# Kernel optimization log

Measured on AMD Instinct MI355X. Metric: run time of the kernel, lower is better.

Reference implementation:

```python
import jax, jax.numpy as jnp
import numpy as np

VOCAB = 1000
HID = 512      # hidden_size == context_size (hidden is initialized to context)
EMB = 512


def setup_inputs() -> dict:
    key = jax.random.key(0)
    ks = jax.random.split(key, 8)
    B = 128
    scale_ih = 1.0 / np.sqrt(HID)
    inp = {
        "context": jax.random.normal(ks[0], (B, HID), dtype=jnp.float32),
        "embed_table": jax.random.normal(ks[1], (VOCAB, EMB), dtype=jnp.float32) * 0.02,
        "W_ih": jax.random.uniform(ks[2], (4 * HID, HID + EMB), minval=-scale_ih, maxval=scale_ih, dtype=jnp.float32),
        "b_ih": jax.random.uniform(ks[3], (4 * HID,), minval=-scale_ih, maxval=scale_ih, dtype=jnp.float32),
        "W_hh": jax.random.uniform(ks[4], (4 * HID, HID), minval=-scale_ih, maxval=scale_ih, dtype=jnp.float32),
        "b_hh": jax.random.uniform(ks[5], (4 * HID,), minval=-scale_ih, maxval=scale_ih, dtype=jnp.float32),
        "W_out": jax.random.uniform(ks[6], (VOCAB, HID), minval=-scale_ih, maxval=scale_ih, dtype=jnp.float32),
        "b_out": jax.random.uniform(ks[7], (VOCAB,), minval=-scale_ih, maxval=scale_ih, dtype=jnp.float32),
        "start_id": 1,
        "max_seq_len": 256,
    }
    return inp


def reference(context, embed_table, W_ih, b_ih, W_hh, b_hh, W_out, b_out, start_id, max_seq_len):
    B = context.shape[0]
    hidden0 = context                                   # torch: hidden = context
    cell0 = jnp.zeros((B, HID), dtype=context.dtype)
    init_emb = jnp.broadcast_to(embed_table[start_id], (B, EMB))

    def step(carry, _):
        h, c, emb = carry
        x = jnp.concatenate([context, emb], axis=1)     # [B, C+E]
        gates = x @ W_ih.T + b_ih + h @ W_hh.T + b_hh   # [B, 4H]
        i_g, f_g, g_g, o_g = jnp.split(gates, 4, axis=1)  # torch LSTMCell gate order
        i_g = jax.nn.sigmoid(i_g)
        f_g = jax.nn.sigmoid(f_g)
        g_g = jnp.tanh(g_g)
        o_g = jax.nn.sigmoid(o_g)
        c_new = f_g * c + i_g * g_g
        h_new = o_g * jnp.tanh(c_new)
        out = h_new @ W_out.T + b_out                   # [B, V]
        next_emb = embed_table[jnp.argmax(out, axis=1)]  # greedy-decode feedback
        return (h_new, c_new, next_emb), out

    (h_f, c_f, _), outs = jax.lax.scan(step, (hidden0, cell0, init_emb), None, length=max_seq_len)
    output_tensor = jnp.transpose(outs, (1, 0, 2))      # [B, T, V]
    return output_tensor, h_f, c_f
```

## Files before the change

### kernel.cpp

```cpp
#include <hip/hip_runtime.h>
#include <float.h>
#include <math.h>

#define B_    128
#define H_    512
#define V_    1000
#define T_    256
#define G4_   2048
#define NBLK  256
#define SPIN_MAX (1 << 17)

#define AT_LOAD(p)    __hip_atomic_load((p), __ATOMIC_RELAXED, __HIP_MEMORY_SCOPE_AGENT)
#define AT_STORE(p,v) __hip_atomic_store((p), (v), __ATOMIC_RELAXED, __HIP_MEMORY_SCOPE_AGENT)

typedef float f2 __attribute__((ext_vector_type(2)));

#define PINF2(v_) asm volatile("" : "+v"(v_))

__device__ __forceinline__ float red4(float x) {
  x += __int_as_float(__builtin_amdgcn_mov_dpp(__float_as_int(x), 0xB1, 0xF, 0xF, true));
  x += __int_as_float(__builtin_amdgcn_mov_dpp(__float_as_int(x), 0x4E, 0xF, 0xF, true));
  return x;
}

__device__ __forceinline__ float fsigmoid(float x) {
  return 1.f / (1.f + __expf(-x));
}
__device__ __forceinline__ float ftanh(float x) {
  const float e = __expf(2.f * fabsf(x));
  return copysignf(1.f - 2.f / (e + 1.f), x);
}

__global__ __launch_bounds__(256) void gemm_nt_k512(
    const float* __restrict__ A, int M,
    const float* __restrict__ Bm, int ldb, int koff,
    const float* __restrict__ bias1, const float* __restrict__ bias2,
    float* __restrict__ C, int ldc, int ileave)
{
  __shared__ float As[16][68];
  __shared__ float Bs[16][68];
  const int tid = threadIdx.x;
  const int m0 = blockIdx.y * 64, n0 = blockIdx.x * 64;
  const int tm = tid & 15, tn = tid >> 4;
  const int lm = tid & 63, kq = tid >> 6;
  float acc[4][4] = {};
  for (int k0 = 0; k0 < 512; k0 += 16) {
    float4 av = make_float4(0.f, 0.f, 0.f, 0.f);
    if (m0 + lm < M) av = *(const float4*)(A + (size_t)(m0 + lm) * 512 + k0 + kq * 4);
    float4 bv = *(const float4*)(Bm + (size_t)(n0 + lm) * ldb + koff + k0 + kq * 4);
    __syncthreads();
    As[kq*4+0][lm] = av.x; As[kq*4+1][lm] = av.y; As[kq*4+2][lm] = av.z; As[kq*4+3][lm] = av.w;
    Bs[kq*4+0][lm] = bv.x; Bs[kq*4+1][lm] = bv.y; Bs[kq*4+2][lm] = bv.z; Bs[kq*4+3][lm] = bv.w;
    __syncthreads();
#pragma unroll
    for (int kk = 0; kk < 16; ++kk) {
      const float4 a = *(const float4*)&As[kk][tm * 4];
      const float4 b = *(const float4*)&Bs[kk][tn * 4];
      const float aa[4] = {a.x, a.y, a.z, a.w};
      const float bb[4] = {b.x, b.y, b.z, b.w};
#pragma unroll
      for (int i = 0; i < 4; ++i)
#pragma unroll
        for (int j = 0; j < 4; ++j)
          acc[i][j] = fmaf(aa[i], bb[j], acc[i][j]);
    }
  }
#pragma unroll
  for (int i = 0; i < 4; ++i) {
    const int m = m0 + tm * 4 + i;
    if (m < M) {
#pragma unroll
      for (int j = 0; j < 4; ++j) {
        const int n = n0 + tn * 4 + j;
        float v = acc[i][j];
        if (bias1) v += bias1[n];
        if (bias2) v += bias2[n];
        const size_t idx = ileave ? ((size_t)m * ldc + (size_t)(n & 511) * 4 + (n >> 9))
                                  : ((size_t)m * ldc + n);
        C[idx] = v;
      }
    }
  }
}

__global__ __launch_bounds__(256) void init_kernel(
    const float* __restrict__ ctx, float* __restrict__ hbuf,
    unsigned long long* __restrict__ amax,
    int* __restrict__ hdone, const int* __restrict__ start_id)
{
  const int i = blockIdx.x * blockDim.x + threadIdx.x;
  ((float4*)(hbuf + B_ * H_))[i] = ((const float4*)ctx)[i];
  if (i < B_ * 32) {
    const int m = i & 31;
    const unsigned long long w = (m == 0)
        ? ((((unsigned long long)__float_as_uint(FLT_MAX)) << 32) |
           (1u << 16) | (unsigned)(*start_id))
        : ((((unsigned long long)__float_as_uint(-FLT_MAX)) << 32) | (1u << 16));
    amax[(size_t)B_ * 32 + i] = w;
  }
  if (i < 2 * 8 * 32) hdone[i * 16] = 0;
}

__global__ __launch_bounds__(512, 2) void decoder_main(
    const float* __restrict__ Whh,
    const float* __restrict__ Wout,
    const float* __restrict__ bout,
    const float* __restrict__ proj,
    const float* __restrict__ basep,
    float* __restrict__ hbuf,
    unsigned long long* __restrict__ amax,
    int* __restrict__ hdone,
    float* __restrict__ out)
{
  __shared__ struct alignas(16) SM {
    float hs[16][640];
    float gbase[16][68];
    float gq[2][16][324];
    float lq[2][16][132];
    float sbout[32];
    int   tok[16];
  } sm;

  const int tid  = threadIdx.x;
  const int bid  = blockIdx.x;
  const int gid  = bid >> 5;
  const int mem  = bid & 31;
  const int lane = tid & 63;
  const int w    = tid >> 6;
  const int row_base = gid * 16;
  const int vb   = mem * 32;

  const int q1  = lane >> 4;
  const int kc  = lane & 15;
  const int i3  = kc & 3;
  const int quad = kc >> 2;
  const int blk = w & 3;
  const int par = w >> 2;
  const int hoff  = par * 256 + kc * 16;
  const int hcol  = (par * 16 + kc) * 20;

  const int goff = (q1 * 4 + i3) * 20 + blk * 4 + quad;
  const int loff = (blk * 8 + q1 * 2 + i3) * 4 + quad;

  f2 w1p[4][8];
#pragma unroll
  for (int i = 0; i < 4; ++i) {
    const f2* p = (const f2*)(Whh + (size_t)(blk * 512 + mem * 16 + q1 * 4 + i) * H_ + hoff);
#pragma unroll
    for (int j = 0; j < 8; ++j) w1p[i][j] = p[j];
  }
  const int v0 = vb + blk * 8 + q1 * 2;
  f2 w2p[2][8];
#pragma unroll
  for (int jj = 0; jj < 2; ++jj) {
    const int vv = (v0 + jj < V_) ? (v0 + jj) : (V_ - 1);
    const f2* p = (const f2*)(Wout + (size_t)vv * H_ + hoff);
#pragma unroll
    for (int j = 0; j < 8; ++j) w2p[jj][j] = p[j];
  }
#pragma unroll
  for (int i = 0; i < 4; ++i)
#pragma unroll
    for (int j = 0; j < 8; ++j) PINF2(w1p[i][j]);
#pragma unroll
  for (int jj = 0; jj < 2; ++jj)
#pragma unroll
    for (int j = 0; j < 8; ++j) PINF2(w2p[jj][j]);

#pragma unroll
  for (int kx = 0; kx < 2; ++kx) {
    const int e = tid + kx * 512;
    const int r = e >> 6, c = e & 63;
    sm.gbase[r][c] = basep[(size_t)(row_base + r) * G4_ + mem * 64 + c];
  }
  if (tid < 32) sm.sbout[tid] = (vb + tid < V_) ? bout[vb + tid] : 0.f;

  float c_reg = 0.f;
  const size_t BTVo = (size_t)B_ * T_ * V_;

  {
    const unsigned long long* hq =
        (const unsigned long long*)(hbuf + (size_t)B_ * H_ + (size_t)row_base * H_);
    unsigned long long v[8];
#pragma unroll
    for (int i = 0; i < 8; ++i) v[i] = AT_LOAD(&hq[tid + i * 512]);
#pragma unroll
    for (int i = 0; i < 8; ++i) {
      const int idx = tid + i * 512;
      const int row = idx >> 8, cp = idx & 255;
      *(unsigned long long*)&sm.hs[row][(cp >> 3) * 20 + (cp & 7) * 2] = v[i];
    }
  }
  __syncthreads();

  for (int t = 0; t < T_; ++t) {
    float* hdst = hbuf + (size_t)(t & 1) * (B_ * H_);

#pragma unroll 2
    for (int r = 0; r < 16; ++r) {
      const f2* hr = (const f2*)&sm.hs[r][hcol];
      f2 c0 = {0.f, 0.f}, c1 = {0.f, 0.f}, c2 = {0.f, 0.f}, c3 = {0.f, 0.f};
#pragma unroll
      for (int j = 0; j < 8; ++j) {
        const f2 hv = hr[j];
        c0 = w1p[0][j] * hv + c0;
        c1 = w1p[1][j] * hv + c1;
        c2 = w1p[2][j] * hv + c2;
        c3 = w1p[3][j] * hv + c3;
      }
      float a0 = c0.x + c0.y;
      float a1 = c1.x + c1.y;
      float a2 = c2.x + c2.y;
      float a3 = c3.x + c3.y;
      a0 = red4(a0); a1 = red4(a1); a2 = red4(a2); a3 = red4(a3);
      const float av = (i3 == 0) ? a0 : (i3 == 1) ? a1 : (i3 == 2) ? a2 : a3;
      sm.gq[par][r][goff] = av;
    }

    {
      const int prow = tid >> 5, pj = tid & 31;
      const unsigned expect = (unsigned)(t + 1) << 16;
      const unsigned long long* ap =
          amax + ((size_t)((t + 1) & 1) * B_ + row_base + prow) * 32;
      unsigned long long wv = AT_LOAD(&ap[pj]);
      for (int it = 0; (((unsigned)wv ^ expect) & 0xFFFF0000u) && it < SPIN_MAX; ++it) {
        __builtin_amdgcn_s_sleep(1);
        wv = AT_LOAD(&ap[pj]);
      }
      __atomic_signal_fence(__ATOMIC_ACQ_REL);
      float v  = __uint_as_float((unsigned)(wv >> 32));
      int   ix = (int)((unsigned)wv & 0xFFFFu);
#pragma unroll
      for (int d = 16; d >= 1; d >>= 1) {
        const float vo = __shfl_xor(v, d, 32);
        const int   io = __shfl_xor(ix, d, 32);
        if (vo > v || (vo == v && io < ix)) { v = vo; ix = io; }
      }
      if (pj == 0) sm.tok[prow] = (ix >= 0 && ix < V_) ? ix : 0;
    }
    __syncthreads();

    if (tid < 256) {
      const int rl = tid >> 4, ul = tid & 15;
      const int tk = sm.tok[rl];
      float gate[4];
#pragma unroll
      for (int g = 0; g < 4; ++g) {
        const float4 qa = *(const float4*)&sm.gq[0][rl][ul * 20 + g * 4];
        const float4 qb = *(const float4*)&sm.gq[1][rl][ul * 20 + g * 4];
        gate[g] = ((qa.x + qa.y) + (qa.z + qa.w)) + ((qb.x + qb.y) + (qb.z + qb.w));
      }
      const float4 gc = *(const float4*)&sm.gbase[rl][ul * 4];
      const float4 gp = *(const float4*)&proj[(size_t)tk * G4_ + (size_t)(mem * 16 + ul) * 4];
      const float gx = gate[0] + gc.x + gp.x;
      const float gy = gate[1] + gc.y + gp.y;
      const float gz = gate[2] + gc.z + gp.z;
      const float gw = gate[3] + gc.w + gp.w;
      const float ig = fsigmoid(gx);
      const float fg = fsigmoid(gy);
      const float gg = ftanh(gz);
      const float og = fsigmoid(gw);
      const float cn = fg * c_reg + ig * gg;
      c_reg = cn;
      const float hn = og * ftanh(cn);
      const int row = row_base + rl, hid = mem * 16 + ul;
      const float hn2 = __shfl_down(hn, 1);
      if ((ul & 1) == 0) {
        const unsigned long long pk =
            (unsigned long long)__float_as_uint(hn) |
            (((unsigned long long)__float_as_uint(hn2)) << 32);
        AT_STORE((unsigned long long*)&hdst[(size_t)row * H_ + hid], pk);
      }
      if (t == T_ - 1) {
        out[BTVo + (size_t)row * H_ + hid] = hn;
        out[BTVo + (size_t)B_ * H_ + (size_t)row * H_ + hid] = cn;
      }
    }
    __syncthreads();
    if (tid == 0)
      AT_STORE(&hdone[(((t & 1) * 8 + gid) * 32 + mem) * 16], t + 2);

    if (tid < 32) {
      int* fp = &hdone[(((t & 1) * 8 + gid) * 32 + tid) * 16];
      for (int it = 0; AT_LOAD(fp) != t + 2 && it < SPIN_MAX; ++it)
        __builtin_amdgcn_s_sleep(1);
    }
    __atomic_signal_fence(__ATOMIC_ACQ_REL);
    __syncthreads();

    {
      const unsigned long long* hq =
          (const unsigned long long*)(hdst + (size_t)row_base * H_);
      unsigned long long v[8];
#pragma unroll
      for (int i = 0; i < 8; ++i) v[i] = AT_LOAD(&hq[tid + i * 512]);
#pragma unroll
      for (int i = 0; i < 8; ++i) {
        const int idx = tid + i * 512;
        const int row = idx >> 8, cp = idx & 255;
        *(unsigned long long*)&sm.hs[row][(cp >> 3) * 20 + (cp & 7) * 2] = v[i];
      }
    }
    __syncthreads();

#pragma unroll 2
    for (int r = 0; r < 16; ++r) {
      const f2* hr = (const f2*)&sm.hs[r][hcol];
      f2 c0 = {0.f, 0.f}, c1 = {0.f, 0.f};
#pragma unroll
      for (int j = 0; j < 8; ++j) {
        const f2 hv = hr[j];
        c0 = w2p[0][j] * hv + c0;
        c1 = w2p[1][j] * hv + c1;
      }
      float b0 = c0.x + c0.y;
      float b1 = c1.x + c1.y;
      b0 = red4(b0); b1 = red4(b1);
      if (i3 < 2)
        sm.lq[par][r][loff] = (i3 == 0) ? b0 : b1;
    }
    __syncthreads();

    {
      const int r = tid >> 5, j = tid & 31;
      const float4 qa = *(const float4*)&sm.lq[0][r][j * 4];
      const float4 qb = *(const float4*)&sm.lq[1][r][j * 4];
      float v = ((qa.x + qa.y) + (qa.z + qa.w)) +
                ((qb.x + qb.y) + (qb.z + qb.w)) + sm.sbout[j];
      if (vb + j < V_)
        out[((size_t)(row_base + r) * T_ + t) * V_ + vb + j] = v;
      else
        v = -FLT_MAX;
      int ix = j;
#pragma unroll
      for (int d = 16; d >= 1; d >>= 1) {
        const float vo = __shfl_xor(v, d, 32);
        const int   io = __shfl_xor(ix, d, 32);
        if (vo > v || (vo == v && io < ix)) { v = vo; ix = io; }
      }
      if (j == 0) {
        const unsigned long long pk =
            (((unsigned long long)__float_as_uint(v)) << 32) |
            ((unsigned)(t + 2) << 16) | (unsigned)(vb + ix);
        AT_STORE(&amax[((size_t)(t & 1) * B_ + row_base + r) * 32 + mem], pk);
      }
    }
  }
}

extern "C" void kernel_launch(void* const* d_in, const int* in_sizes, int n_in,
                              void* d_out, int out_size, void* d_ws, size_t ws_size,
                              hipStream_t stream)
{
  const float* ctx   = (const float*)d_in[0];
  const float* emb   = (const float*)d_in[1];
  const float* Wih   = (const float*)d_in[2];
  const float* bih   = (const float*)d_in[3];
  const float* Whh   = (const float*)d_in[4];
  const float* bhh   = (const float*)d_in[5];
  const float* Wout  = (const float*)d_in[6];
  const float* bout  = (const float*)d_in[7];
  const int*   start = (const int*)d_in[8];
  float* out = (float*)d_out;

  char* ws = (char*)d_ws;
  float* proj  = (float*)(ws + 0);
  float* basep = (float*)(ws + 8192000);
  float* hbuf  = (float*)(ws + 9240576);
  unsigned long long* amax = (unsigned long long*)(ws + 9764864);
  int*   hdone = (int*)(ws + 9830400);

  hipLaunchKernelGGL(gemm_nt_k512, dim3(32, 2), dim3(256), 0, stream,
                     ctx, B_, Wih, 1024, 0, bih, bhh, basep, G4_, 1);
  hipLaunchKernelGGL(gemm_nt_k512, dim3(32, 16), dim3(256), 0, stream,
                     emb, V_, Wih, 1024, 512, (const float*)nullptr, (const float*)nullptr,
                     proj, G4_, 1);
  hipLaunchKernelGGL(init_kernel, dim3(64), dim3(256), 0, stream,
                     ctx, hbuf, amax, hdone, start);

  void* args[] = {(void*)&Whh, (void*)&Wout, (void*)&bout, (void*)&proj, (void*)&basep,
                  (void*)&hbuf, (void*)&amax, (void*)&hdone, (void*)&out};
  hipLaunchCooperativeKernel(reinterpret_cast<const void*>(decoder_main),
                             dim3(NBLK), dim3(512), args, 0, stream);
}
```

Before: 2.696 ms.

## Replace per-step hidden-state barrier with tagged hidden values polled directly

Each hidden-state value is now stored as a 64-bit word carrying the float and a step tag. Consumers spin on the tags of the data they need, so the separate hdone flag write, the flag spin and two block-wide barriers go away. The token-dependent projection row is also fetched into shared memory during the argmax phase instead of after the barrier. In exchange the hidden-state traffic doubles, since each value now takes 8 bytes, and the poll loop runs per element.

Result: slower. 3.838 ms (+42.4%).

```diff
diff --git a/kernel.cpp b/kernel.cpp
--- a/kernel.cpp
+++ b/kernel.cpp
@@ -9,6 +9,8 @@
 #define G4_   2048
 #define NBLK  256
 #define SPIN_MAX (1 << 17)
+
+typedef unsigned long long ull;
 
 #define AT_LOAD(p)    __hip_atomic_load((p), __ATOMIC_RELAXED, __HIP_MEMORY_SCOPE_AGENT)
 #define AT_STORE(p,v) __hip_atomic_store((p), (v), __ATOMIC_RELAXED, __HIP_MEMORY_SCOPE_AGENT)
@@ -84,21 +86,24 @@
 }
 
 __global__ __launch_bounds__(256) void init_kernel(
-    const float* __restrict__ ctx, float* __restrict__ hbuf,
-    unsigned long long* __restrict__ amax,
-    int* __restrict__ hdone, const int* __restrict__ start_id)
+    const float* __restrict__ ctx, ull* __restrict__ hx,
+    ull* __restrict__ amax, const int* __restrict__ start_id)
 {
   const int i = blockIdx.x * blockDim.x + threadIdx.x;
-  ((float4*)(hbuf + B_ * H_))[i] = ((const float4*)ctx)[i];
+#pragma unroll
+  for (int k = 0; k < 4; ++k) {
+    const int j = i + k * 16384;
+    hx[(size_t)B_ * H_ + j] =
+        (((ull)__float_as_uint(ctx[j])) << 32) | 1u;
+    hx[j] = 0ull;
+  }
   if (i < B_ * 32) {
     const int m = i & 31;
-    const unsigned long long w = (m == 0)
-        ? ((((unsigned long long)__float_as_uint(FLT_MAX)) << 32) |
-           (1u << 16) | (unsigned)(*start_id))
-        : ((((unsigned long long)__float_as_uint(-FLT_MAX)) << 32) | (1u << 16));
-    amax[(size_t)B_ * 32 + i] = w;
-  }
-  if (i < 2 * 8 * 32) hdone[i * 16] = 0;
+    amax[(size_t)B_ * 32 + i] = (m == 0)
+        ? ((((ull)__float_as_uint(FLT_MAX)) << 32) | (1u << 16) | (unsigned)(*start_id))
+        : ((((ull)__float_as_uint(-FLT_MAX)) << 32) | (1u << 16));
+    amax[i] = ((ull)__float_as_uint(-FLT_MAX)) << 32;
+  }
 }
 
 __global__ __launch_bounds__(512, 2) void decoder_main(
@@ -107,18 +112,17 @@
     const float* __restrict__ bout,
     const float* __restrict__ proj,
     const float* __restrict__ basep,
-    float* __restrict__ hbuf,
-    unsigned long long* __restrict__ amax,
-    int* __restrict__ hdone,
+    ull* __restrict__ hx,
+    ull* __restrict__ amax,
     float* __restrict__ out)
 {
   __shared__ struct alignas(16) SM {
     float hs[16][640];
     float gbase[16][68];
+    float gproj[16][68];
     float gq[2][16][324];
     float lq[2][16][132];
     float sbout[32];
-    int   tok[16];
   } sm;
 
   const int tid  = threadIdx.x;
@@ -138,6 +142,7 @@
   const int par = w >> 2;
   const int hoff  = par * 256 + kc * 16;
   const int hcol  = (par * 16 + kc) * 20;
+  const int scol  = (tid >> 4) * 20 + (tid & 15);
 
   const int goff = (q1 * 4 + i3) * 20 + blk * 4 + quad;
   const int loff = (blk * 8 + q1 * 2 + i3) * 4 + quad;
@@ -179,22 +184,18 @@
   const size_t BTVo = (size_t)B_ * T_ * V_;
 
   {
-    const unsigned long long* hq =
-        (const unsigned long long*)(hbuf + (size_t)B_ * H_ + (size_t)row_base * H_);
-    unsigned long long v[8];
-#pragma unroll
-    for (int i = 0; i < 8; ++i) v[i] = AT_LOAD(&hq[tid + i * 512]);
-#pragma unroll
-    for (int i = 0; i < 8; ++i) {
-      const int idx = tid + i * 512;
-      const int row = idx >> 8, cp = idx & 255;
-      *(unsigned long long*)&sm.hs[row][(cp >> 3) * 20 + (cp & 7) * 2] = v[i];
-    }
+    const ull* hq = hx + (size_t)B_ * H_ + (size_t)row_base * H_;
+    ull v[16];
+#pragma unroll
+    for (int i = 0; i < 16; ++i) v[i] = AT_LOAD(&hq[i * 512 + tid]);
+#pragma unroll
+    for (int i = 0; i < 16; ++i)
+      sm.hs[i][scol] = __uint_as_float((unsigned)(v[i] >> 32));
   }
   __syncthreads();
 
   for (int t = 0; t < T_; ++t) {
-    float* hdst = hbuf + (size_t)(t & 1) * (B_ * H_);
+    ull* hxw = hx + (size_t)(t & 1) * (B_ * H_);
 
 #pragma unroll 2
     for (int r = 0; r < 16; ++r) {
@@ -220,9 +221,9 @@
     {
       const int prow = tid >> 5, pj = tid & 31;
       const unsigned expect = (unsigned)(t + 1) << 16;
-      const unsigned long long* ap =
+      const ull* ap =
           amax + ((size_t)((t + 1) & 1) * B_ + row_base + prow) * 32;
-      unsigned long long wv = AT_LOAD(&ap[pj]);
+      ull wv = AT_LOAD(&ap[pj]);
       for (int it = 0; (((unsigned)wv ^ expect) & 0xFFFF0000u) && it < SPIN_MAX; ++it) {
         __builtin_amdgcn_s_sleep(1);
         wv = AT_LOAD(&ap[pj]);
@@ -236,13 +237,17 @@
         const int   io = __shfl_xor(ix, d, 32);
         if (vo > v || (vo == v && io < ix)) { v = vo; ix = io; }
       }
-      if (pj == 0) sm.tok[prow] = (ix >= 0 && ix < V_) ? ix : 0;
+      const int tk = (ix >= 0 && ix < V_) ? ix : 0;
+      if (pj < 16) {
+        const float4 gp = *(const float4*)&proj[(size_t)tk * G4_ +
+                                                (size_t)(mem * 16 + pj) * 4];
+        *(float4*)&sm.gproj[prow][pj * 4] = gp;
+      }
     }
     __syncthreads();
 
     if (tid < 256) {
       const int rl = tid >> 4, ul = tid & 15;
-      const int tk = sm.tok[rl];
       float gate[4];
 #pragma unroll
       for (int g = 0; g < 4; ++g) {
@@ -251,7 +256,7 @@
         gate[g] = ((qa.x + qa.y) + (qa.z + qa.w)) + ((qb.x + qb.y) + (qb.z + qb.w));
       }
       const float4 gc = *(const float4*)&sm.gbase[rl][ul * 4];
-      const float4 gp = *(const float4*)&proj[(size_t)tk * G4_ + (size_t)(mem * 16 + ul) * 4];
+      const float4 gp = *(const float4*)&sm.gproj[rl][ul * 4];
       const float gx = gate[0] + gc.x + gp.x;
       const float gy = gate[1] + gc.y + gp.y;
       const float gz = gate[2] + gc.z + gp.z;
@@ -264,42 +269,33 @@
       c_reg = cn;
       const float hn = og * ftanh(cn);
       const int row = row_base + rl, hid = mem * 16 + ul;
-      const float hn2 = __shfl_down(hn, 1);
-      if ((ul & 1) == 0) {
-        const unsigned long long pk =
-            (unsigned long long)__float_as_uint(hn) |
-            (((unsigned long long)__float_as_uint(hn2)) << 32);
-        AT_STORE((unsigned long long*)&hdst[(size_t)row * H_ + hid], pk);
-      }
+      AT_STORE(&hxw[(size_t)row * H_ + hid],
+               (((ull)__float_as_uint(hn)) << 32) | (unsigned)(t + 2));
       if (t == T_ - 1) {
         out[BTVo + (size_t)row * H_ + hid] = hn;
         out[BTVo + (size_t)B_ * H_ + (size_t)row * H_ + hid] = cn;
       }
     }
-    __syncthreads();
-    if (tid == 0)
-      AT_STORE(&hdone[(((t & 1) * 8 + gid) * 32 + mem) * 16], t + 2);
-
-    if (tid < 32) {
-      int* fp = &hdone[(((t & 1) * 8 + gid) * 32 + tid) * 16];
-      for (int it = 0; AT_LOAD(fp) != t + 2 && it < SPIN_MAX; ++it)
-        __builtin_amdgcn_s_sleep(1);
-    }
-    __atomic_signal_fence(__ATOMIC_ACQ_REL);
-    __syncthreads();
 
     {
-      const unsigned long long* hq =
-          (const unsigned long long*)(hdst + (size_t)row_base * H_);
-      unsigned long long v[8];
-#pragma unroll
-      for (int i = 0; i < 8; ++i) v[i] = AT_LOAD(&hq[tid + i * 512]);
-#pragma unroll
-      for (int i = 0; i < 8; ++i) {
-        const int idx = tid + i * 512;
-        const int row = idx >> 8, cp = idx & 255;
-        *(unsigned long long*)&sm.hs[row][(cp >> 3) * 20 + (cp & 7) * 2] = v[i];
-      }
+      const ull* hq = hxw + (size_t)row_base * H_;
+      const unsigned tagv = (unsigned)(t + 2);
+      ull v[16];
+#pragma unroll
+      for (int i = 0; i < 16; ++i) v[i] = AT_LOAD(&hq[i * 512 + tid]);
+#pragma unroll
+      for (int i = 0; i < 16; ++i) {
+        int it = 0;
+        while ((unsigned)v[i] != tagv && it < SPIN_MAX) {
+          __builtin_amdgcn_s_sleep(1);
+          v[i] = AT_LOAD(&hq[i * 512 + tid]);
+          ++it;
+        }
+      }
+      __atomic_signal_fence(__ATOMIC_ACQ_REL);
+#pragma unroll
+      for (int i = 0; i < 16; ++i)
+        sm.hs[i][scol] = __uint_as_float((unsigned)(v[i] >> 32));
     }
     __syncthreads();
 
@@ -339,8 +335,8 @@
         if (vo > v || (vo == v && io < ix)) { v = vo; ix = io; }
       }
       if (j == 0) {
-        const unsigned long long pk =
-            (((unsigned long long)__float_as_uint(v)) << 32) |
+        const ull pk =
+            (((ull)__float_as_uint(v)) << 32) |
             ((unsigned)(t + 2) << 16) | (unsigned)(vb + ix);
         AT_STORE(&amax[((size_t)(t & 1) * B_ + row_base + r) * 32 + mem], pk);
       }
@@ -366,9 +362,8 @@
   char* ws = (char*)d_ws;
   float* proj  = (float*)(ws + 0);
   float* basep = (float*)(ws + 8192000);
-  float* hbuf  = (float*)(ws + 9240576);
-  unsigned long long* amax = (unsigned long long*)(ws + 9764864);
-  int*   hdone = (int*)(ws + 9830400);
+  ull*   hx    = (ull*)(ws + 9240576);
+  ull*   amax  = (ull*)(ws + 10289152);
 
   hipLaunchKernelGGL(gemm_nt_k512, dim3(32, 2), dim3(256), 0, stream,
                      ctx, B_, Wih, 1024, 0, bih, bhh, basep, G4_, 1);
@@ -376,10 +371,10 @@
                      emb, V_, Wih, 1024, 512, (const float*)nullptr, (const float*)nullptr,
                      proj, G4_, 1);
   hipLaunchKernelGGL(init_kernel, dim3(64), dim3(256), 0, stream,
-                     ctx, hbuf, amax, hdone, start);
+                     ctx, hx, amax, start);
 
   void* args[] = {(void*)&Whh, (void*)&Wout, (void*)&bout, (void*)&proj, (void*)&basep,
-                  (void*)&hbuf, (void*)&amax, (void*)&hdone, (void*)&out};
+                  (void*)&hx, (void*)&amax, (void*)&out};
   hipLaunchCooperativeKernel(reinterpret_cast<const void*>(decoder_main),
                              dim3(NBLK), dim3(512), args, 0, stream);
 }
```
